# Performance work log

Hardware: AMD Instinct MI355X
Metric: run time of the kernel (lower is better)

The kernel has to match this reference:

```python
import jax, jax.numpy as jnp
import numpy as np

B, T, D, H = 32, 2048, 256, 256


def setup_inputs() -> dict:
    key = jax.random.key(0)
    ks = jax.random.split(key, 7)
    stdv = 1.0 / float(np.sqrt(H))
    u = lambda k, shape: jax.random.uniform(k, shape, jnp.float32, -stdv, stdv)
    return {
        "x": jax.random.normal(ks[0], (B, T, D), jnp.float32),
        # gate order along the 4H axis: i, f, c, o (stacked = same math as 4 separate matmuls)
        "W_f": u(ks[1], (D, 4 * H)),
        "U_f": u(ks[2], (H, 4 * H)),
        "b_f": u(ks[3], (4 * H,)),
        "W_b": u(ks[4], (D, 4 * H)),
        "U_b": u(ks[5], (H, 4 * H)),
        "b_b": u(ks[6], (4 * H,)),
    }


def _bilstm(x, W_f, U_f, b_f, W_b, U_b, b_b):
    Bk = x.shape[0]
    Hh = U_f.shape[0]
    # precompute input projections for all timesteps (one big GEMM per direction)
    xw_f = jnp.einsum('btd,dg->tbg', x, W_f) + b_f            # [T,B,4H]
    xw_b = jnp.einsum('btd,dg->tbg', x[:, ::-1], W_b) + b_b   # time-reversed input
    h0 = jnp.zeros((Bk, Hh), x.dtype)
    carry0 = (h0, h0, h0, h0)  # h, c, h_back, c_back

    def step(carry, inp):
        h, c, hb, cb = carry
        gw, gwb = inp  # [B,4H] each
        # NOTE: original module applies sigmoid to ALL four gates (incl. candidate g)
        g = jax.nn.sigmoid(gw + h @ U_f)
        i, f, gg, o = jnp.split(g, 4, axis=-1)
        c = f + c + i * gg          # faithful: additive forget term
        h = o + jnp.tanh(c)         # faithful: additive output term
        gb = jax.nn.sigmoid(gwb + hb @ U_b)
        ib, fb, ggb, ob = jnp.split(gb, 4, axis=-1)
        cb = fb + cb + ib * ggb
        hb = ob + jnp.tanh(cb)
        return (h, c, hb, cb), (h, hb)

    (h, c, hb, cb), (hs, hbs) = jax.lax.scan(step, carry0, (xw_f, xw_b))
    hs = jnp.transpose(hs, (1, 0, 2))              # [B,T,H]
    hbs = jnp.transpose(hbs, (1, 0, 2))[:, ::-1]   # flip back to forward time order
    y_net = jnp.concatenate([hs, hbs], axis=2)     # [B,T,2H]
    y_t = jnp.concatenate([h, hb], axis=1)         # [B,2H]
    return y_t, y_net


def reference(x, W_f, U_f, b_f, W_b, U_b, b_b):
    return _bilstm(x, W_f, U_f, b_f, W_b, U_b, b_b)
```

## Files before the change

### kernel.cpp

```cpp
#include <hip/hip_runtime.h>
#include <stdint.h>


#define TT 2048

typedef __attribute__((ext_vector_type(8))) short  short8;
typedef __attribute__((ext_vector_type(8))) __bf16 bf16x8;
typedef __attribute__((ext_vector_type(4))) float  f32x4;
typedef __attribute__((ext_vector_type(4))) int    i32x4;

#define XW_BYTES    (2ull*TT*32*1024*2)
#define STAGE_BYTES (2ull*TT*32*256*2)

__device__ __forceinline__ unsigned short f2bf(float x){
  uint32_t u = __float_as_uint(x);
  return (unsigned short)((u + 0x7fffu + ((u>>16)&1u)) >> 16);
}
__device__ __forceinline__ float bf2f(unsigned short h){
  return __uint_as_float(((uint32_t)h)<<16);
}

__global__ __launch_bounds__(512, 2)
void k_xw(const float* __restrict__ x, const float* __restrict__ Wf,
          const float* __restrict__ Wb, const float* __restrict__ bf,
          const float* __restrict__ bb, uint16_t* __restrict__ xw)
{
  __shared__ uint16_t wt[1024*32];
  const int bid = blockIdx.x;
  const int d   = bid >> 10;
  const int t0  = (bid & 1023) * 2;
  const float* __restrict__ W    = d ? Wb : Wf;
  const float* __restrict__ bias = d ? bb : bf;
  const int tid  = threadIdx.x;
  const int lane = tid & 63;
  const int wv   = tid >> 6;
  const int mt   = wv >> 1;
  const int nh   = wv & 1;
  const int l15  = lane & 15, lg = lane >> 4;

  f32x4 acc[32];
#pragma unroll
  for (int i=0;i<32;i++) acc[i] = (f32x4){0.f,0.f,0.f,0.f};

  const int arow = mt*16 + l15;
  const int ab   = arow & 31;
  const int atl  = arow >> 5;
  const float* __restrict__ xrow = x + ((size_t)ab*TT + (t0+atl))*256;

  for (int kc = 0; kc < 8; ++kc) {
    const int k0 = kc*32;
    __syncthreads();
#pragma unroll
    for (int cc=0; cc<2; ++cc){
      const int c = tid + cc*512;
      union { unsigned short s[32]; short8 v8[4]; } u;
#pragma unroll
      for (int j=0;j<32;j++) u.s[j] = f2bf(W[(size_t)(k0+j)*1024 + c]);
      short8* dst = (short8*)&wt[c*32];
#pragma unroll
      for (int o=0;o<4;o++) dst[o ^ (c&3)] = u.v8[o];
    }
    __syncthreads();
    union { unsigned short s[8]; short8 v; } af;
    {
      const float4 a0 = *(const float4*)&xrow[k0 + lg*8];
      const float4 a1 = *(const float4*)&xrow[k0 + lg*8 + 4];
      af.s[0]=f2bf(a0.x); af.s[1]=f2bf(a0.y); af.s[2]=f2bf(a0.z); af.s[3]=f2bf(a0.w);
      af.s[4]=f2bf(a1.x); af.s[5]=f2bf(a1.y); af.s[6]=f2bf(a1.z); af.s[7]=f2bf(a1.w);
    }
#pragma unroll
    for (int nt=0; nt<32; ++nt){
      const int ct = nh*512 + nt*16 + l15;
      short8 bfr = *(const short8*)&wt[ct*32 + ((lg ^ (ct&3))<<3)];
      acc[nt] = __builtin_amdgcn_mfma_f32_16x16x32_bf16(
        __builtin_bit_cast(bf16x8, af.v), __builtin_bit_cast(bf16x8, bfr), acc[nt], 0,0,0);
    }
  }
#pragma unroll
  for (int nt=0; nt<32; ++nt){
    const int c = nh*512 + nt*16 + l15;
    const int gate = c >> 8, hc = c & 255;
    const float bv = bias[c];
#pragma unroll
    for (int q=0;q<4;q++){
      const int row = mt*16 + lg*4 + q;
      const int b = row & 31, tl = row >> 5;
      xw[((size_t)(d*TT + t0 + tl)*32 + b)*1024 + hc*4 + gate] = f2bf(acc[nt][q] + bv);
    }
  }
}

__global__ __launch_bounds__(1024)
void k_rec(const float* __restrict__ Uf, const float* __restrict__ Ub,
           const uint16_t* __restrict__ xw, uint16_t* __restrict__ stage,
           float* __restrict__ out)
{
  const int bid = blockIdx.x;
  const int d   = bid >> 3;
  const int bs  = bid & 7;
  const int tid  = threadIdx.x;
  const int lane = tid & 63;
  const int w    = tid >> 6;
  const int l15  = lane & 15, lg = lane >> 4;
  const int cb   = lane & 3;
  const int hx   = lane >> 2;
  const int gb   = bs*4 + cb;

  const float* __restrict__ U = d ? Ub : Uf;

  __shared__ i32x4 pre16[16*64];
  __shared__ __align__(16) unsigned char hlds[2][1024];

  i32x4 aU[4][4];
#pragma unroll
  for (int q=0;q<4;q++){
    const int g = q*256 + w*16 + l15;
#pragma unroll
    for (int m=0;m<4;m++){
      uint32_t rg[4] = {0,0,0,0};
#pragma unroll
      for (int jj=0;jj<16;jj++){
        const int k = m*64 + lg*16 + jj;
        float u = U[(size_t)k*1024 + g];
        int v = __float2int_rn(u * 2032.0f);
        v = v > 127 ? 127 : (v < -127 ? -127 : v);
        rg[jj>>2] |= (uint32_t)(v & 255) << ((jj&3)*8);
      }
      aU[q][m] = (i32x4){(int)rg[0],(int)rg[1],(int)rg[2],(int)rg[3]};
    }
  }

  ((uint16_t*)hlds)[tid] = 0;
  __syncthreads();

  const float DQ = 1.0f / (2032.0f * 63.5f);
  float cs = 0.f, hcur = 0.f;

  auto gwload = [&](int t)->uint64_t {
    int tt = t < TT ? t : TT-1;
    int tg = d ? (TT-1-tt) : tt;
    return *(const uint64_t*)(xw + (((size_t)(d*TT + tg)*32 + gb)<<10) + (w*16+hx)*4);
  };
  uint64_t gw0 = gwload(0), gw1 = gwload(1);

  for (int t = 0; t < TT; t += 2) {
#pragma unroll
    for (int half = 0; half < 2; ++half) {
      const int tc  = t + half;
      const int pin = half;

      i32x4 acc[4];
#pragma unroll
      for (int q=0;q<4;q++) acc[q] = (i32x4){0,0,0,0};
      {
        const unsigned char* hb = &hlds[pin][cb*256];
#pragma unroll
        for (int m=0;m<4;m++){
          i32x4 hf = *(const i32x4*)(hb + ((m*64 + lg*16) ^ (cb<<4)));
#pragma unroll
          for (int q=0;q<4;q++)
            acc[q] = __builtin_amdgcn_mfma_i32_16x16x64_i8(aU[q][m], hf, acc[q], 0,0,0);
        }
      }
      if (l15 < 4){
#pragma unroll
        for (int r=0;r<4;r++){
          i32x4 v = (i32x4){acc[0][r], acc[1][r], acc[2][r], acc[3][r]};
          pre16[w*64 + l15*16 + ((lg*4 + r + 2*l15) & 15)] = v;
        }
      }
      asm volatile("s_waitcnt lgkmcnt(0)" ::: "memory");
      __builtin_amdgcn_sched_barrier(0);

      i32x4 pv = pre16[w*64 + cb*16 + ((hx + 2*cb) & 15)];
      const uint64_t gwc = half ? gw1 : gw0;
      float pr[4];
#pragma unroll
      for (int q=0;q<4;q++)
        pr[q] = (float)pv[q]*DQ + bf2f((unsigned short)(gwc >> (q*16)));
      float si = __builtin_amdgcn_rcpf(1.0f + __expf(-pr[0]));
      float sf = __builtin_amdgcn_rcpf(1.0f + __expf(-pr[1]));
      float sg = __builtin_amdgcn_rcpf(1.0f + __expf(-pr[2]));
      float so = __builtin_amdgcn_rcpf(1.0f + __expf(-pr[3]));
      cs = sf + cs + si*sg;
      float th = 1.0f - 2.0f*__builtin_amdgcn_rcpf(1.0f + __expf(2.0f*cs));
      hcur = so + th;

      int q8 = (int)(hcur * 63.5f + 0.5f); q8 = q8 > 127 ? 127 : q8;
      hlds[pin^1][cb*256 + ((w*16 + hx) ^ (cb<<4))] = (unsigned char)q8;

      {
        const int tg = d ? (TT-1-tc) : tc;
        stage[(((size_t)(d*TT + tg)*32 + gb)<<8) + w*16 + hx] = f2bf(hcur);
      }
      if (half) gw1 = gwload(tc+2); else gw0 = gwload(tc+2);

      asm volatile("s_waitcnt lgkmcnt(0)" ::: "memory");
      __builtin_amdgcn_sched_barrier(0);
      __builtin_amdgcn_s_barrier();
      __builtin_amdgcn_sched_barrier(0);
    }
  }

  out[(size_t)gb*512 + d*256 + w*16 + hx] = hcur;
}

__global__ __launch_bounds__(256)
void k_out(const uint16_t* __restrict__ stage, float* __restrict__ y_net)
{
  const int blk = blockIdx.x;
  const int b = blk >> 11;
  const int t = blk & 2047;
  const int tid = threadIdx.x;
  const uint16_t v0 = stage[((size_t)(0*TT + t)*32 + b)*256 + tid];
  const uint16_t v1 = stage[((size_t)(1*TT + t)*32 + b)*256 + tid];
  float* o = y_net + ((size_t)b*TT + t)*512;
  o[tid]       = bf2f(v0);
  o[tid + 256] = bf2f(v1);
}

extern "C" void kernel_launch(void* const* d_in, const int* in_sizes, int n_in,
                              void* d_out, int out_size, void* d_ws, size_t ws_size,
                              hipStream_t stream)
{
  const float* x  = (const float*)d_in[0];
  const float* Wf = (const float*)d_in[1];
  const float* Uf = (const float*)d_in[2];
  const float* bf = (const float*)d_in[3];
  const float* Wb = (const float*)d_in[4];
  const float* Ub = (const float*)d_in[5];
  const float* bb = (const float*)d_in[6];
  float* out = (float*)d_out;
  uint8_t* ws = (uint8_t*)d_ws;
  uint16_t* xw    = (uint16_t*)ws;
  uint16_t* stage = (uint16_t*)(ws + XW_BYTES);

  k_xw <<<dim3(2048),    dim3(512),  0, stream>>>(x, Wf, Wb, bf, bb, xw);
  k_rec<<<dim3(16),      dim3(1024), 0, stream>>>(Uf, Ub, xw, stage, out);
  k_out<<<dim3(32*2048), dim3(256),  0, stream>>>(stage, out + 32*512);
}
```

Measured before the change: 2.704 ms.

## Pre-convert W to bf16, coalesce xw stores, and use bpermute gate gather

Adds a small kernel that converts and transposes the input-projection weights to bf16 once, so each k_xw block copies ready-made bf16 rows instead of converting strided fp32 loads. The xw epilogue is staged through LDS so it can write contiguous 128-bit rows in place of scattered 2-byte stores. In the recurrent kernel, the LDS round-trip used to gather gate pre-activations is replaced with ds_bpermute lane shuffles. The same kernel also merges the i*g sigmoid product into one reciprocal, walks the xw and stage addresses with pointer increments, and sets wave priorities. These cut the per-step latency of the serial loop at the cost of extra workspace and one more launch.

Result: slower. 3.669 ms (+35.7%).

```diff
diff --git a/kernel.cpp b/kernel.cpp
--- a/kernel.cpp
+++ b/kernel.cpp
@@ -11,6 +11,7 @@
 
 #define XW_BYTES    (2ull*TT*32*1024*2)
 #define STAGE_BYTES (2ull*TT*32*256*2)
+#define WBF_BYTES   (2ull*1024*256*2)
 
 __device__ __forceinline__ unsigned short f2bf(float x){
   uint32_t u = __float_as_uint(x);
@@ -20,16 +21,31 @@
   return __uint_as_float(((uint32_t)h)<<16);
 }
 
+__global__ __launch_bounds__(256)
+void k_wq(const float* __restrict__ Wf, const float* __restrict__ Wb,
+          uint16_t* __restrict__ wbf)
+{
+  const int d  = blockIdx.x >> 3;
+  const int kc = blockIdx.x & 7;
+  const float* __restrict__ W = d ? Wb : Wf;
+  const int tid = threadIdx.x;
+  for (int ii = 0; ii < 128; ++ii){
+    const int idx = ii*256 + tid;
+    const int k = idx >> 10, c = idx & 1023;
+    wbf[((size_t)(d*1024 + c) << 8) + kc*32 + k] =
+        f2bf(W[(size_t)(kc*32 + k)*1024 + c]);
+  }
+}
+
 __global__ __launch_bounds__(512, 2)
-void k_xw(const float* __restrict__ x, const float* __restrict__ Wf,
-          const float* __restrict__ Wb, const float* __restrict__ bf,
-          const float* __restrict__ bb, uint16_t* __restrict__ xw)
+void k_xw(const float* __restrict__ x, const uint16_t* __restrict__ wbf,
+          const float* __restrict__ bf, const float* __restrict__ bb,
+          uint16_t* __restrict__ xw)
 {
   __shared__ uint16_t wt[1024*32];
   const int bid = blockIdx.x;
   const int d   = bid >> 10;
   const int t0  = (bid & 1023) * 2;
-  const float* __restrict__ W    = d ? Wb : Wf;
   const float* __restrict__ bias = d ? bb : bf;
   const int tid  = threadIdx.x;
   const int lane = tid & 63;
@@ -53,12 +69,11 @@
 #pragma unroll
     for (int cc=0; cc<2; ++cc){
       const int c = tid + cc*512;
-      union { unsigned short s[32]; short8 v8[4]; } u;
-#pragma unroll
-      for (int j=0;j<32;j++) u.s[j] = f2bf(W[(size_t)(k0+j)*1024 + c]);
+      const uint16_t* wsrc = wbf + ((size_t)(d*1024 + c) << 8) + k0;
       short8* dst = (short8*)&wt[c*32];
 #pragma unroll
-      for (int o=0;o<4;o++) dst[o ^ (c&3)] = u.v8[o];
+      for (int o=0;o<4;o++)
+        dst[o ^ (c&3)] = *(const short8*)(wsrc + o*8);
     }
     __syncthreads();
     union { unsigned short s[8]; short8 v; } af;
@@ -76,21 +91,39 @@
         __builtin_bit_cast(bf16x8, af.v), __builtin_bit_cast(bf16x8, bfr), acc[nt], 0,0,0);
     }
   }
-#pragma unroll
-  for (int nt=0; nt<32; ++nt){
-    const int c = nh*512 + nt*16 + l15;
-    const int gate = c >> 8, hc = c & 255;
-    const float bv = bias[c];
-#pragma unroll
-    for (int q=0;q<4;q++){
-      const int row = mt*16 + lg*4 + q;
-      const int b = row & 31, tl = row >> 5;
-      xw[((size_t)(d*TT + t0 + tl)*32 + b)*1024 + hc*4 + gate] = f2bf(acc[nt][q] + bv);
-    }
-  }
-}
-
-__global__ __launch_bounds__(1024)
+  uint16_t* wt2 = wt;
+#pragma unroll
+  for (int R=0; R<2; ++R){
+    __syncthreads();
+    if ((mt >> 1) == R){
+#pragma unroll
+      for (int nt=0; nt<32; ++nt){
+        const int c = nh*512 + nt*16 + l15;
+        const int s = ((c & 255) << 2) | (c >> 8);
+        const float bv = bias[c];
+#pragma unroll
+        for (int q=0;q<4;q++){
+          const int row = mt*16 + lg*4 + q;
+          wt2[(row - R*32)*1024 + s] = f2bf(acc[nt][q] + bv);
+        }
+      }
+    }
+    __syncthreads();
+    {
+      const int row = tid >> 4;
+      const int seg = tid & 15;
+      const int arow2 = R*32 + row;
+      const int b = arow2 & 31, tl = arow2 >> 5;
+      uint16_t* dst = xw + ((size_t)(d*TT + t0 + tl)*32 + b)*1024 + seg*64;
+      const uint16_t* srcl = wt2 + row*1024 + seg*64;
+#pragma unroll
+      for (int o=0;o<8;o++)
+        *(int4*)(dst + o*8) = *(const int4*)(srcl + o*8);
+    }
+  }
+}
+
+__global__ __launch_bounds__(1024, 1)
 void k_rec(const float* __restrict__ Uf, const float* __restrict__ Ub,
            const uint16_t* __restrict__ xw, uint16_t* __restrict__ stage,
            float* __restrict__ out)
@@ -108,7 +141,6 @@
 
   const float* __restrict__ U = d ? Ub : Uf;
 
-  __shared__ i32x4 pre16[16*64];
   __shared__ __align__(16) unsigned char hlds[2][1024];
 
   i32x4 aU[4][4];
@@ -130,79 +162,84 @@
     }
   }
 
-  ((uint16_t*)hlds)[tid] = 0;
+  if (tid < 512) ((uint32_t*)hlds)[tid] = 0u;
   __syncthreads();
 
+  const int slot = w >> 2;
+  if (slot == 0) __builtin_amdgcn_s_setprio(2);
+  else if (slot == 1) __builtin_amdgcn_s_setprio(1);
+
+  const int bpi = ((((lane >> 4) << 4) | cb) << 2);
+  const int selA = hx & 1, selB = hx & 2;
   const float DQ = 1.0f / (2032.0f * 63.5f);
-  float cs = 0.f, hcur = 0.f;
-
-  auto gwload = [&](int t)->uint64_t {
-    int tt = t < TT ? t : TT-1;
-    int tg = d ? (TT-1-tt) : tt;
-    return *(const uint64_t*)(xw + (((size_t)(d*TT + tg)*32 + gb)<<10) + (w*16+hx)*4);
-  };
-  uint64_t gw0 = gwload(0), gw1 = gwload(1);
-
-  for (int t = 0; t < TT; t += 2) {
-#pragma unroll
-    for (int half = 0; half < 2; ++half) {
-      const int tc  = t + half;
-      const int pin = half;
-
-      i32x4 acc[4];
-#pragma unroll
-      for (int q=0;q<4;q++) acc[q] = (i32x4){0,0,0,0};
-      {
-        const unsigned char* hb = &hlds[pin][cb*256];
-#pragma unroll
-        for (int m=0;m<4;m++){
-          i32x4 hf = *(const i32x4*)(hb + ((m*64 + lg*16) ^ (cb<<4)));
-#pragma unroll
-          for (int q=0;q<4;q++)
-            acc[q] = __builtin_amdgcn_mfma_i32_16x16x64_i8(aU[q][m], hf, acc[q], 0,0,0);
-        }
+
+  const long xstep = (d ? -1 : 1) * (long)(32*1024);
+  const long sstep = (d ? -1 : 1) * (long)(32*256);
+  const int tg0 = d ? TT-1 : 0;
+  const uint16_t* px = xw + ((size_t)(d*TT + tg0)*32 + gb)*1024 + (w*16+hx)*4;
+  uint16_t* ps = stage + ((size_t)(d*TT + tg0)*32 + gb)*256 + (w*16+hx);
+  uint64_t gw0 = *(const uint64_t*)px; px += xstep;
+  uint64_t gw1 = *(const uint64_t*)px; px += xstep;
+
+  float cs = 0.f, hv = 0.f;
+
+  for (int t = 0; t < TT; ++t) {
+    const int p = t & 1;
+
+    i32x4 acc[4];
+#pragma unroll
+    for (int q=0;q<4;q++) acc[q] = (i32x4){0,0,0,0};
+    {
+      const unsigned char* hb = &hlds[p][cb*256];
+#pragma unroll
+      for (int m=0;m<4;m++){
+        i32x4 hf = *(const i32x4*)(hb + ((m*64 + lg*16) ^ (cb<<4)));
+#pragma unroll
+        for (int q=0;q<4;q++)
+          acc[q] = __builtin_amdgcn_mfma_i32_16x16x64_i8(aU[q][m], hf, acc[q], 0,0,0);
       }
-      if (l15 < 4){
-#pragma unroll
-        for (int r=0;r<4;r++){
-          i32x4 v = (i32x4){acc[0][r], acc[1][r], acc[2][r], acc[3][r]};
-          pre16[w*64 + l15*16 + ((lg*4 + r + 2*l15) & 15)] = v;
-        }
-      }
-      asm volatile("s_waitcnt lgkmcnt(0)" ::: "memory");
-      __builtin_amdgcn_sched_barrier(0);
-
-      i32x4 pv = pre16[w*64 + cb*16 + ((hx + 2*cb) & 15)];
-      const uint64_t gwc = half ? gw1 : gw0;
-      float pr[4];
-#pragma unroll
-      for (int q=0;q<4;q++)
-        pr[q] = (float)pv[q]*DQ + bf2f((unsigned short)(gwc >> (q*16)));
-      float si = __builtin_amdgcn_rcpf(1.0f + __expf(-pr[0]));
-      float sf = __builtin_amdgcn_rcpf(1.0f + __expf(-pr[1]));
-      float sg = __builtin_amdgcn_rcpf(1.0f + __expf(-pr[2]));
-      float so = __builtin_amdgcn_rcpf(1.0f + __expf(-pr[3]));
-      cs = sf + cs + si*sg;
-      float th = 1.0f - 2.0f*__builtin_amdgcn_rcpf(1.0f + __expf(2.0f*cs));
-      hcur = so + th;
-
-      int q8 = (int)(hcur * 63.5f + 0.5f); q8 = q8 > 127 ? 127 : q8;
-      hlds[pin^1][cb*256 + ((w*16 + hx) ^ (cb<<4))] = (unsigned char)q8;
-
-      {
-        const int tg = d ? (TT-1-tc) : tc;
-        stage[(((size_t)(d*TT + tg)*32 + gb)<<8) + w*16 + hx] = f2bf(hcur);
-      }
-      if (half) gw1 = gwload(tc+2); else gw0 = gwload(tc+2);
-
-      asm volatile("s_waitcnt lgkmcnt(0)" ::: "memory");
-      __builtin_amdgcn_sched_barrier(0);
-      __builtin_amdgcn_s_barrier();
-      __builtin_amdgcn_sched_barrier(0);
-    }
-  }
-
-  out[(size_t)gb*512 + d*256 + w*16 + hx] = hcur;
+    }
+
+    int pre[4];
+#pragma unroll
+    for (int q=0;q<4;q++){
+      int p0 = __builtin_amdgcn_ds_bpermute(bpi, acc[q][0]);
+      int p1 = __builtin_amdgcn_ds_bpermute(bpi, acc[q][1]);
+      int p2 = __builtin_amdgcn_ds_bpermute(bpi, acc[q][2]);
+      int p3 = __builtin_amdgcn_ds_bpermute(bpi, acc[q][3]);
+      int s01 = selA ? p1 : p0;
+      int s23 = selA ? p3 : p2;
+      pre[q] = selB ? s23 : s01;
+    }
+
+    const uint64_t gwc = p ? gw1 : gw0;
+    float pr[4];
+#pragma unroll
+    for (int q=0;q<4;q++)
+      pr[q] = fmaf((float)pre[q], DQ, bf2f((unsigned short)(gwc >> (q*16))));
+    float ea = __expf(-pr[0]);
+    float eg = __expf(-pr[2]);
+    float ig = __builtin_amdgcn_rcpf(1.0f + ea + eg + ea*eg);
+    float sf = __builtin_amdgcn_rcpf(1.0f + __expf(-pr[1]));
+    float so = __builtin_amdgcn_rcpf(1.0f + __expf(-pr[3]));
+    cs = sf + cs + ig;
+    float th = 1.0f - 2.0f*__builtin_amdgcn_rcpf(1.0f + __expf(2.0f*cs));
+    hv = so + th;
+
+    int q8 = (int)(hv * 63.5f + 0.5f); q8 = q8 > 127 ? 127 : q8;
+    hlds[p^1][cb*256 + ((w*16 + hx) ^ (cb<<4))] = (unsigned char)q8;
+
+    *ps = f2bf(hv); ps += sstep;
+    if (p) gw1 = *(const uint64_t*)px; else gw0 = *(const uint64_t*)px;
+    if (t < TT-3) px += xstep;
+
+    asm volatile("s_waitcnt lgkmcnt(0)" ::: "memory");
+    __builtin_amdgcn_sched_barrier(0);
+    __builtin_amdgcn_s_barrier();
+    __builtin_amdgcn_sched_barrier(0);
+  }
+
+  out[(size_t)gb*512 + d*256 + w*16 + hx] = hv;
 }
 
 __global__ __launch_bounds__(256)
@@ -234,8 +271,10 @@
   uint8_t* ws = (uint8_t*)d_ws;
   uint16_t* xw    = (uint16_t*)ws;
   uint16_t* stage = (uint16_t*)(ws + XW_BYTES);
-
-  k_xw <<<dim3(2048),    dim3(512),  0, stream>>>(x, Wf, Wb, bf, bb, xw);
+  uint16_t* wbf   = (uint16_t*)(ws + XW_BYTES + STAGE_BYTES);
+
+  k_wq <<<dim3(16),      dim3(256),  0, stream>>>(Wf, Wb, wbf);
+  k_xw <<<dim3(2048),    dim3(512),  0, stream>>>(x, wbf, bf, bb, xw);
   k_rec<<<dim3(16),      dim3(1024), 0, stream>>>(Uf, Ub, xw, stage, out);
   k_out<<<dim3(32*2048), dim3(256),  0, stream>>>(stage, out + 32*512);
 }
```
